# Kernel optimization log

Measured on AMD Instinct MI355X. Metric: run time of the kernel, lower is better.

The kernel has to match this reference:

```python
import jax, jax.numpy as jnp
import numpy as np

POS_INF = 64500.0
B, P, C = 32, 2048, 256
D = C // 2


def setup_inputs() -> dict:
    key = jax.random.key(0)
    ks = jax.random.split(key, 8)
    x = jax.random.normal(ks[0], (B, P, C), dtype=jnp.float32)
    mask = jax.random.randint(ks[1], (B, P), 0, 2).astype(jnp.float32)
    s = 0.05
    Wq = jax.random.normal(ks[2], (C, D), dtype=jnp.float32) * s
    bq = jnp.zeros((D,), dtype=jnp.float32)
    Wk = jax.random.normal(ks[3], (C, D), dtype=jnp.float32) * s
    bk = jnp.zeros((D,), dtype=jnp.float32)
    Wv = jax.random.normal(ks[4], (C, C), dtype=jnp.float32) * s
    bv = jnp.zeros((C,), dtype=jnp.float32)
    return {"x": x, "mask": mask, "Wq": Wq, "bq": bq, "Wk": Wk, "bk": bk, "Wv": Wv, "bv": bv}


def reference(x, mask, Wq, bq, Wk, bk, Wv, bv):
    # Projections (torch Linear: x @ W^T + b; weights here stored [in, out])
    q = x @ Wq + bq          # [B, P, D]
    k = x @ Wk + bk          # [B, P, D]
    v = x @ Wv + bv          # [B, P, C]
    scale = 1.0 / (D ** 0.5)
    attn = jnp.einsum('bpd,bqd->bpq', q, k) * scale   # [B, P, P]
    # additive mask bias broadcast over keys (masks query rows, as in source)
    bias = (mask[:, :, None] - 1.0) * POS_INF          # [B, P, 1]
    attn = jax.nn.softmax(attn + bias, axis=-1)
    out = jnp.einsum('bpq,bqc->bpc', attn, v)          # [B, P, C]
    return out * mask[:, :, None]
```

## Files before the change

### kernel.cpp

```cpp
#include <hip/hip_runtime.h>
#include <hip/hip_bf16.h>

typedef __attribute__((ext_vector_type(8))) short short8;
typedef __attribute__((ext_vector_type(4))) float f32x4;
typedef unsigned int u32;
typedef __attribute__((address_space(3))) u32 lds_u32;
typedef const __attribute__((address_space(1))) u32 glb_u32;

#define NB 32
#define NP 2048
#define NC 256
#define ND 128

#define QSCALE (0.08838834764831845f * 1.4426950408889634f)
#define DEFER_THR 8.0f

__device__ inline float fast_exp2(float x){ return exp2f(x); }

__device__ inline unsigned short f2bf(float f){
  union { float f; unsigned u; } v; v.f = f;
  unsigned r = v.u + 0x7FFFu + ((v.u >> 16) & 1u);
  return (unsigned short)(r >> 16);
}
__device__ inline unsigned pk2(float a, float b){
  return (unsigned)f2bf(a) | ((unsigned)f2bf(b) << 16);
}
__device__ inline unsigned cvtpk(float a, float b){
  unsigned r;
  asm("v_cvt_pk_bf16_f32 %0, %1, %2" : "=v"(r) : "v"(a), "v"(b));
  return r;
}

__global__ __launch_bounds__(256) void prep_w(const float* __restrict__ Wq, const float* __restrict__ bq,
    const float* __restrict__ Wk, const float* __restrict__ bk,
    const float* __restrict__ Wv, const float* __restrict__ bv,
    unsigned short* __restrict__ WqkT, unsigned short* __restrict__ WvT, float* __restrict__ bqk){
  int o = blockIdx.x; int i = threadIdx.x;
  float wqk = (o < ND) ? Wq[i*ND + o] * QSCALE : Wk[i*ND + (o-ND)];
  WqkT[o*NC + i] = f2bf(wqk);
  WvT[o*NC + i]  = f2bf(Wv[i*NC + o]);
  if (i == 0) bqk[o] = (o < ND) ? bq[o]*QSCALE : bk[o-ND];
}

__global__ __launch_bounds__(256) void qkv_proj(const float* __restrict__ x,
    const unsigned short* __restrict__ WqkT, const float* __restrict__ bqk,
    const unsigned short* __restrict__ WvT, const float* __restrict__ bv,
    unsigned short* __restrict__ QK, unsigned short* __restrict__ VT){
  __shared__ unsigned short Alds[64*264];
  const int tid = threadIdx.x;
  const long rowbase = (long)blockIdx.x * 64;
  const int b = blockIdx.x >> 5, pt = blockIdx.x & 31;
  #pragma unroll
  for (int it = 0; it < 16; ++it){
    int chunk = tid + it*256;
    int r = chunk >> 6;
    int c4 = (chunk & 63) << 2;
    const float4 v = *(const float4*)(x + (rowbase + r)*NC + c4);
    *(uint2*)(&Alds[r*264 + c4]) = make_uint2(pk2(v.x, v.y), pk2(v.z, v.w));
  }
  __syncthreads();
  const int w = tid >> 6, lane = tid & 63, g = lane >> 4, c0 = lane & 15;
  const f32x4 zero = {0.f,0.f,0.f,0.f};

  {
    const int wrow = (w >> 1) * 32, wcol = (w & 1) * 128;
    f32x4 acc[2][8];
    #pragma unroll
    for (int m=0;m<2;m++){ for(int n=0;n<8;n++) acc[m][n] = zero; }
    #pragma unroll
    for (int ks=0; ks<8; ++ks){
      short8 a[2], bfr[8];
      #pragma unroll
      for (int m=0;m<2;m++)
        a[m] = *(const short8*)(&Alds[(wrow + 16*m + c0)*264 + ks*32 + 8*g]);
      #pragma unroll
      for (int n=0;n<8;n++)
        bfr[n] = *(const short8*)(&WqkT[(wcol + 16*n + c0)*NC + ks*32 + 8*g]);
      #pragma unroll
      for (int m=0;m<2;m++){
        #pragma unroll
        for(int n=0;n<8;n++)
          acc[m][n] = __builtin_amdgcn_mfma_f32_16x16x32_bf16(a[m], bfr[n], acc[m][n], 0,0,0);
      }
    }
    #pragma unroll
    for (int n=0;n<8;n++){
      int o = wcol + 16*n + c0;
      float bia = bqk[o];
      #pragma unroll
      for (int m=0;m<2;m++){
        long row = rowbase + wrow + 16*m + 4*g;
        #pragma unroll
        for (int r=0;r<4;r++)
          QK[(row + r)*NC + o] = f2bf(acc[m][n][r] + bia);
      }
    }
  }

  {
    const int wc = (w >> 1) * 128, wp = (w & 1) * 32;
    f32x4 acc[8][2];
    #pragma unroll
    for (int m=0;m<8;m++){ for(int n=0;n<2;n++) acc[m][n] = zero; }
    #pragma unroll
    for (int ks=0; ks<8; ++ks){
      short8 a[8], bb[2];
      #pragma unroll
      for (int m=0;m<8;m++)
        a[m] = *(const short8*)(&WvT[(wc + 16*m + c0)*NC + ks*32 + 8*g]);
      #pragma unroll
      for (int n=0;n<2;n++)
        bb[n] = *(const short8*)(&Alds[(wp + 16*n + c0)*264 + ks*32 + 8*g]);
      #pragma unroll
      for (int m=0;m<8;m++){
        #pragma unroll
        for(int n=0;n<2;n++)
          acc[m][n] = __builtin_amdgcn_mfma_f32_16x16x32_bf16(a[m], bb[n], acc[m][n], 0,0,0);
      }
    }
    #pragma unroll
    for (int m=0;m<8;m++){
      int cout = wc + 16*m + 4*g;
      #pragma unroll
      for (int r=0;r<4;r++){
        float bia = bv[cout + r];
        long base = ((long)b*NC + cout + r)*NP + pt*64 + wp;
        #pragma unroll
        for (int n=0;n<2;n++)
          VT[base + 16*n + c0] = f2bf(acc[m][n][r] + bia);
      }
    }
  }
}

__global__ __launch_bounds__(256,2) void attn(const unsigned short* __restrict__ QK,
    const unsigned short* __restrict__ VT, const float* __restrict__ mask,
    float* __restrict__ out){
  __shared__ unsigned short Klds[64*128];
  __shared__ unsigned short Vlds[256*64];
  __shared__ unsigned short Plds[4*32*72];
  const int tid = threadIdx.x;
  const int b = blockIdx.x >> 4, qt = blockIdx.x & 15;
  const int qbase = qt * 128;
  const int w = tid >> 6, lane = tid & 63, g = lane >> 4, c0 = lane & 15;
  const int c07 = (c0 & 7) << 3;
  unsigned short* pw = &Plds[w * 2304];

  const long qrow0 = (long)b * NP + qbase + w*32;
  short8 qf[2][4];
  #pragma unroll
  for (int n2=0;n2<2;n2++)
    #pragma unroll
    for (int ks=0; ks<4; ++ks)
      qf[n2][ks] = *(const short8*)(&QK[(qrow0 + n2*16 + c0)*NC + ks*32 + 8*g]);

  const f32x4 zero = {0.f,0.f,0.f,0.f};
  f32x4 oacc[2][16];
  #pragma unroll
  for (int n2=0;n2<2;n2++){ for (int n=0;n<16;n++) oacc[n2][n] = zero; }
  float m_run[2] = {-1e30f, -1e30f}, l_run[2] = {0.f, 0.f};
  const long kvbase = (long)b * NP;
  const long vtbase = (long)b * NC * NP;

  for (int t=0; t<32; ++t){
    const int kb = t*64;
    __syncthreads();
    #pragma unroll
    for (int j=0;j<4;++j){
      int chunk = w*256 + j*64 + lane;
      int key = chunk >> 4, sp = chunk & 15;
      const unsigned short* src = &QK[(kvbase + kb + key)*NC + ND + ((sp ^ (key&7))*8)];
      __builtin_amdgcn_global_load_lds((glb_u32*)src, (lds_u32*)&Klds[(w*256 + j*64)*8], 16, 0, 0);
    }
    #pragma unroll
    for (int j=0;j<8;++j){
      int chunk = w*512 + j*64 + lane;
      int crow = chunk >> 3, sp = chunk & 7;
      const unsigned short* src = &VT[vtbase + (long)crow*NP + kb + ((sp ^ (crow&7))*8)];
      __builtin_amdgcn_global_load_lds((glb_u32*)src, (lds_u32*)&Vlds[(w*512 + j*64)*8], 16, 0, 0);
    }
    __syncthreads();

    f32x4 st[4][2];
    #pragma unroll
    for (int m=0;m<4;m++){ st[m][0] = zero; st[m][1] = zero; }
    __builtin_amdgcn_s_setprio(1);
    #pragma unroll
    for (int ks=0;ks<4;ks++){
      short8 ka[4];
      #pragma unroll
      for (int m=0;m<4;m++)
        ka[m] = *(const short8*)(&Klds[(16*m + c0)*128 + ((ks*32 + 8*g) ^ c07)]);
      #pragma unroll
      for (int m=0;m<4;m++){
        st[m][0] = __builtin_amdgcn_mfma_f32_16x16x32_bf16(ka[m], qf[0][ks], st[m][0], 0,0,0);
        st[m][1] = __builtin_amdgcn_mfma_f32_16x16x32_bf16(ka[m], qf[1][ks], st[m][1], 0,0,0);
      }
    }
    __builtin_amdgcn_s_setprio(0);

    #pragma unroll
    for (int n2=0;n2<2;n2++){
      float tm = st[0][n2][0];
      #pragma unroll
      for (int m=0;m<4;m++){
        #pragma unroll
        for (int r=0;r<4;r++) tm = fmaxf(tm, st[m][n2][r]);
      }
      tm = fmaxf(tm, __shfl_xor(tm, 16));
      tm = fmaxf(tm, __shfl_xor(tm, 32));
      if (!__all(tm <= m_run[n2] + DEFER_THR)){
        float mn = fmaxf(m_run[n2], tm);
        float alpha = fast_exp2(m_run[n2] - mn);
        l_run[n2] *= alpha;
        m_run[n2] = mn;
        float ar[4];
        #pragma unroll
        for (int r=0;r<4;r++) ar[r] = __shfl(alpha, 4*g + r);
        #pragma unroll
        for (int n=0;n<16;n++){
          #pragma unroll
          for (int r=0;r<4;r++) oacc[n2][n][r] *= ar[r];
        }
      }
      const float mr = m_run[n2];
      float psum = 0.f;
      #pragma unroll
      for (int m=0;m<4;m++){
        float p0 = fast_exp2(st[m][n2][0] - mr);
        float p1 = fast_exp2(st[m][n2][1] - mr);
        float p2 = fast_exp2(st[m][n2][2] - mr);
        float p3 = fast_exp2(st[m][n2][3] - mr);
        psum += (p0 + p1) + (p2 + p3);
        uint2 pd;
        pd.x = cvtpk(p0, p1);
        pd.y = cvtpk(p2, p3);
        *(uint2*)(&pw[(n2*16 + c0)*72 + 16*m + 4*g]) = pd;
      }
      psum += __shfl_xor(psum, 16);
      psum += __shfl_xor(psum, 32);
      l_run[n2] += psum;
    }

    __builtin_amdgcn_s_setprio(1);
    #pragma unroll
    for (int kk=0;kk<2;kk++){
      short8 pa[2];
      pa[0] = *(const short8*)(&pw[(c0     )*72 + kk*32 + 8*g]);
      pa[1] = *(const short8*)(&pw[(16 + c0)*72 + kk*32 + 8*g]);
      #pragma unroll
      for (int n=0;n<16;n++){
        short8 vb = *(const short8*)(&Vlds[(16*n + c0)*64 + ((kk*32 + 8*g) ^ c07)]);
        oacc[0][n] = __builtin_amdgcn_mfma_f32_16x16x32_bf16(pa[0], vb, oacc[0][n], 0,0,0);
        oacc[1][n] = __builtin_amdgcn_mfma_f32_16x16x32_bf16(pa[1], vb, oacc[1][n], 0,0,0);
      }
    }
    __builtin_amdgcn_s_setprio(0);
  }

  #pragma unroll
  for (int n2=0;n2<2;n2++){
    float fac[4];
    #pragma unroll
    for (int r=0;r<4;r++){
      float lr = __shfl(l_run[n2], 4*g + r);
      long q = qbase + w*32 + n2*16 + 4*g + r;
      fac[r] = mask[(long)b*NP + q] / lr;
    }
    #pragma unroll
    for (int n=0;n<16;n++){
      #pragma unroll
      for (int r=0;r<4;r++){
        long q = qbase + w*32 + n2*16 + 4*g + r;
        out[((long)b*NP + q)*NC + 16*n + c0] = oacc[n2][n][r] * fac[r];
      }
    }
  }
}

extern "C" void kernel_launch(void* const* d_in, const int* in_sizes, int n_in,
                              void* d_out, int out_size, void* d_ws, size_t ws_size,
                              hipStream_t stream){
  const float* x    = (const float*)d_in[0];
  const float* mask = (const float*)d_in[1];
  const float* Wq   = (const float*)d_in[2];
  const float* bq   = (const float*)d_in[3];
  const float* Wk   = (const float*)d_in[4];
  const float* bk   = (const float*)d_in[5];
  const float* Wv   = (const float*)d_in[6];
  const float* bv   = (const float*)d_in[7];
  float* outp = (float*)d_out;
  char* ws = (char*)d_ws;

  unsigned short* QK   = (unsigned short*)(ws);
  unsigned short* VT   = (unsigned short*)(ws + 33554432);
  char* scratch        = (char*)d_out;
  unsigned short* WqkT = (unsigned short*)(scratch);
  unsigned short* WvT  = (unsigned short*)(scratch + 131072);
  float* bqk           = (float*)(scratch + 262144);

  prep_w  <<<256, 256, 0, stream>>>(Wq, bq, Wk, bk, Wv, bv, WqkT, WvT, bqk);
  qkv_proj<<<1024, 256, 0, stream>>>(x, WqkT, bqk, WvT, bv, QK, VT);
  attn    <<<512, 256, 0, stream>>>(QK, VT, mask, outp);
}
```

Baseline: 208.8 us.

## Alias P buffer onto K tile in LDS to fit three blocks per CU

```diff
diff --git a/kernel.cpp b/kernel.cpp
--- a/kernel.cpp
+++ b/kernel.cpp
@@ -133,18 +133,17 @@
   }
 }
 
-__global__ __launch_bounds__(256,2) void attn(const unsigned short* __restrict__ QK,
+__global__ __launch_bounds__(256,3) void attn(const unsigned short* __restrict__ QK,
     const unsigned short* __restrict__ VT, const float* __restrict__ mask,
     float* __restrict__ out){
   __shared__ unsigned short Klds[64*128];
   __shared__ unsigned short Vlds[256*64];
-  __shared__ unsigned short Plds[4*32*72];
   const int tid = threadIdx.x;
   const int b = blockIdx.x >> 4, qt = blockIdx.x & 15;
   const int qbase = qt * 128;
   const int w = tid >> 6, lane = tid & 63, g = lane >> 4, c0 = lane & 15;
   const int c07 = (c0 & 7) << 3;
-  unsigned short* pw = &Plds[w * 2304];
+  unsigned short* pw = &Klds[w * 2048];
 
   const long qrow0 = (long)b * NP + qbase + w*32;
   short8 qf[2][4];
@@ -227,27 +226,38 @@
       float psum = 0.f;
       #pragma unroll
       for (int m=0;m<4;m++){
-        float p0 = fast_exp2(st[m][n2][0] - mr);
-        float p1 = fast_exp2(st[m][n2][1] - mr);
-        float p2 = fast_exp2(st[m][n2][2] - mr);
-        float p3 = fast_exp2(st[m][n2][3] - mr);
-        psum += (p0 + p1) + (p2 + p3);
-        uint2 pd;
-        pd.x = cvtpk(p0, p1);
-        pd.y = cvtpk(p2, p3);
-        *(uint2*)(&pw[(n2*16 + c0)*72 + 16*m + 4*g]) = pd;
+        #pragma unroll
+        for (int r=0;r<4;r++){
+          float p = fast_exp2(st[m][n2][r] - mr);
+          st[m][n2][r] = p; psum += p;
+        }
       }
       psum += __shfl_xor(psum, 16);
       psum += __shfl_xor(psum, 32);
       l_run[n2] += psum;
     }
 
+    __syncthreads();
+
+    #pragma unroll
+    for (int n2=0;n2<2;n2++){
+      const int prow = n2*16 + c0;
+      const int pxor = (prow & 7) << 3;
+      #pragma unroll
+      for (int m=0;m<4;m++){
+        uint2 pd;
+        pd.x = cvtpk(st[m][n2][0], st[m][n2][1]);
+        pd.y = cvtpk(st[m][n2][2], st[m][n2][3]);
+        *(uint2*)(&pw[prow*64 + ((16*m + 4*g) ^ pxor)]) = pd;
+      }
+    }
+
     __builtin_amdgcn_s_setprio(1);
     #pragma unroll
     for (int kk=0;kk<2;kk++){
       short8 pa[2];
-      pa[0] = *(const short8*)(&pw[(c0     )*72 + kk*32 + 8*g]);
-      pa[1] = *(const short8*)(&pw[(16 + c0)*72 + kk*32 + 8*g]);
+      pa[0] = *(const short8*)(&pw[(c0     )*64 + ((kk*32 + 8*g) ^ ((c0&7)<<3))]);
+      pa[1] = *(const short8*)(&pw[(16 + c0)*64 + ((kk*32 + 8*g) ^ ((c0&7)<<3))]);
       #pragma unroll
       for (int n=0;n<16;n++){
         short8 vb = *(const short8*)(&Vlds[(16*n + c0)*64 + ((kk*32 + 8*g) ^ c07)]);
```

Result: slower. 640.6 us (+206.8%).
